# Optimization experiments

Measured on AMD Instinct MI355X. Metric: run time of the kernel, lower is better.

## Reference

```python
import jax, jax.numpy as jnp
import numpy as np

B, S, D, H = 2, 2048, 1024, 16
DK = D // H


def setup_inputs() -> dict:
    key = jax.random.key(0)
    ks = jax.random.split(key, 11)
    def lin(k):
        kw, kb = jax.random.split(k)
        bound = 1.0 / np.sqrt(D)
        w = jax.random.uniform(kw, (D, D), jnp.float32, -bound, bound)
        b = jax.random.uniform(kb, (D,), jnp.float32, -bound, bound)
        return w, b
    wq_w, wq_b = lin(ks[0])
    wk_w, wk_b = lin(ks[1])
    wv_w, wv_b = lin(ks[2])
    wo_w, wo_b = lin(ks[3])
    q = jax.random.normal(ks[4], (B, S, D), jnp.float32)
    k = jax.random.normal(ks[5], (B, S, D), jnp.float32)
    v = jax.random.normal(ks[6], (B, S, D), jnp.float32)
    # causal mask, broadcastable to (B, H, S, S); 0 -> masked
    mask = jnp.tril(jnp.ones((S, S), jnp.int32))[None, None, :, :]
    return {"q": q, "k": k, "v": v, "mask": mask,
            "wq_w": wq_w, "wq_b": wq_b, "wk_w": wk_w, "wk_b": wk_b,
            "wv_w": wv_w, "wv_b": wv_b, "wo_w": wo_w, "wo_b": wo_b}


def reference(q, k, v, mask, wq_w, wq_b, wk_w, wk_b, wv_w, wv_b, wo_w, wo_b):
    # projections (torch Linear: x @ W^T + b)
    def split_heads(x):  # (B,S,D) -> (B,H,S,DK)
        return x.reshape(B, S, H, DK).transpose(0, 2, 1, 3)
    Q = split_heads(q @ wq_w.T + wq_b)
    K = split_heads(k @ wk_w.T + wk_b)
    V = split_heads(v @ wv_w.T + wv_b)
    scores = jnp.einsum('bhqd,bhkd->bhqk', Q, K) / np.sqrt(DK).astype(np.float32)
    scores = jnp.where(mask == 0, jnp.float32(-1e9), scores)
    attn = jax.nn.softmax(scores, axis=-1)
    out = jnp.einsum('bhqk,bhkd->bhqd', attn, V)  # (B,H,S,DK)
    out = out.transpose(0, 2, 1, 3).reshape(B, S, D)
    return out @ wo_w.T + wo_b
```

## Files before the change

kernel.cpp:

```cpp
#include <hip/hip_runtime.h>

#define DEV __device__ __forceinline__

typedef __attribute__((ext_vector_type(8))) short short8;
typedef __attribute__((ext_vector_type(4))) float f32x4;
typedef __bf16 bf16x8 __attribute__((ext_vector_type(8)));
typedef unsigned int u32;
typedef unsigned short u16;

constexpr int Bb = 2, Ss = 2048, Dd = 1024, Hh = 16, DKc = 64;
constexpr int Kk = 1024;

#define QSCALE 0.1803368801111204f

DEV u16 f2bf(float f) {
  u32 u = __builtin_bit_cast(u32, f);
  u32 r = (u + 0x7fffu + ((u >> 16) & 1u)) >> 16;
  return (u16)r;
}

DEV u32 pk_bf16(float lo, float hi) {
  u32 w;
  asm("v_cvt_pk_bf16_f32 %0, %1, %2" : "=v"(w) : "v"(lo), "v"(hi));
  return w;
}

DEV f32x4 mfma16(short8 a, short8 b, f32x4 c) {
  return __builtin_amdgcn_mfma_f32_16x16x32_bf16(
      __builtin_bit_cast(bf16x8, a), __builtin_bit_cast(bf16x8, b), c, 0, 0, 0);
}

DEV void gload_lds16(const u16* g, u16* lds) {
  __builtin_amdgcn_global_load_lds(
      (const __attribute__((address_space(1))) u32*)g,
      (__attribute__((address_space(3))) u32*)lds, 16, 0, 0);
}

struct CvtArgs {
  const float* in[7];
  u16* out[7];
  int n[7];
};

__global__ __launch_bounds__(256) void cvt_all(CvtArgs a) {
  int z = blockIdx.z;
  int i = (blockIdx.x * 256 + threadIdx.x) * 4;
  if (i >= a.n[z]) return;
  float4 v = *reinterpret_cast<const float4*>(a.in[z] + i);
  ushort4 o;
  o.x = f2bf(v.x); o.y = f2bf(v.y); o.z = f2bf(v.z); o.w = f2bf(v.w);
  *reinterpret_cast<ushort4*>(a.out[z] + i) = o;
}

template<int MT, int NT>
DEV void gemm_core(const u16* __restrict__ A, const u16* __restrict__ Bt,
                   u16* smA, u16* smB, f32x4 (&acc)[MT][NT], int gm0, int gn0) {
  constexpr int NSTEP = Kk / 32;
  constexpr int SA = MT * 1024;
  constexpr int SB = NT * 1024;
  constexpr int S = MT / 2 + NT / 2;
  const int tid = threadIdx.x;
  const int w = tid >> 6, l = tid & 63;
  const int g = (l >> 4) & 3, r = l & 15;
  const int wm = w >> 1, wn = w & 1;
  const int srow = l >> 2, scol = (l & 3) * 8;

  auto stage = [&](int buf, int kt) {
    int kb = kt * 32;
#pragma unroll
    for (int cc = 0; cc < MT / 2; ++cc) {
      int c = w + cc * 4;
      gload_lds16(A + (size_t)(gm0 + c * 16 + srow) * Kk + kb + scol,
                  smA + buf * SA + c * 512);
    }
#pragma unroll
    for (int cc = 0; cc < NT / 2; ++cc) {
      int c = w + cc * 4;
      gload_lds16(Bt + (size_t)(gn0 + c * 16 + srow) * Kk + kb + scol,
                  smB + buf * SB + c * 512);
    }
  };

  stage(0, 0);
  stage(1, 1);
  for (int kt = 0; kt < NSTEP; ++kt) {
    const int buf = kt % 3;
    if (kt + 1 < NSTEP) {
      if constexpr (S == 4) asm volatile("s_waitcnt vmcnt(4)" ::: "memory");
      else                  asm volatile("s_waitcnt vmcnt(3)" ::: "memory");
    } else {
      asm volatile("s_waitcnt vmcnt(0)" ::: "memory");
    }
    __builtin_amdgcn_s_barrier();
    __builtin_amdgcn_sched_barrier(0);
    if (kt + 2 < NSTEP) stage((kt + 2) % 3, kt + 2);

    short8 af[MT], bf_[NT];
#pragma unroll
    for (int t = 0; t < MT; ++t)
      af[t] = *reinterpret_cast<const short8*>(
          smA + buf * SA + (wm * (MT * 16) + t * 16 + r) * 32 + g * 8);
#pragma unroll
    for (int t = 0; t < NT; ++t)
      bf_[t] = *reinterpret_cast<const short8*>(
          smB + buf * SB + (wn * (NT * 16) + t * 16 + r) * 32 + g * 8);
    __builtin_amdgcn_s_setprio(1);
#pragma unroll
    for (int mt = 0; mt < MT; ++mt)
#pragma unroll
      for (int nt = 0; nt < NT; ++nt)
        acc[mt][nt] = mfma16(af[mt], bf_[nt], acc[mt][nt]);
    __builtin_amdgcn_s_setprio(0);
  }
}

__global__ __launch_bounds__(256, 3) void proj_qkv(
    const u16* __restrict__ xq, const u16* __restrict__ xk, const u16* __restrict__ xv,
    const u16* __restrict__ Wq, const u16* __restrict__ Wk, const u16* __restrict__ Wv,
    const float* __restrict__ bq, const float* __restrict__ bk, const float* __restrict__ bv,
    u16* __restrict__ Qh, u16* __restrict__ Kh, u16* __restrict__ Vt) {
  __shared__ u16 smA[3 * 128 * 32], smB[3 * 128 * 32];
  const int flat = (blockIdx.z * 32 + blockIdx.y) * 8 + blockIdx.x;
  const int nid = (flat & 7) * 96 + (flat >> 3);
  const int bx = nid & 7, by = (nid >> 3) & 31, z = nid >> 8;
  const u16* A = z == 0 ? xq : (z == 1 ? xk : xv);
  const u16* W = z == 0 ? Wq : (z == 1 ? Wk : Wv);
  const float* bias = z == 0 ? bq : (z == 1 ? bk : bv);
  u16* out = z == 0 ? Qh : (z == 1 ? Kh : Vt);
  const float sc = z == 0 ? QSCALE : 1.0f;
  const int gm0 = by * 128, gn0 = bx * 128;
  f32x4 acc[4][4] = {};
  gemm_core<4, 4>(A, W, smA, smB, acc, gm0, gn0);

  const int tid = threadIdx.x;
  const int w = tid >> 6, l = tid & 63, g = (l >> 4) & 3, r = l & 15;
  const int wm = w >> 1, wn = w & 1;
#pragma unroll
  for (int mt = 0; mt < 4; ++mt) {
#pragma unroll
    for (int nt = 0; nt < 4; ++nt) {
      int ncol = gn0 + wn * 64 + nt * 16 + r;
      int h = ncol >> 6, dk = ncol & 63;
      float bb = bias[ncol];
      int mrow0 = gm0 + wm * 64 + mt * 16 + g * 4;
      int b = mrow0 >> 11, s0 = mrow0 & 2047;
      if (z < 2) {
#pragma unroll
        for (int i = 0; i < 4; ++i)
          out[(((size_t)b * Hh + h) * Ss + s0 + i) * DKc + dk] =
              f2bf((acc[mt][nt][i] + bb) * sc);
      } else {
        ushort4 ov;
        ov.x = f2bf(acc[mt][nt][0] + bb);
        ov.y = f2bf(acc[mt][nt][1] + bb);
        ov.z = f2bf(acc[mt][nt][2] + bb);
        ov.w = f2bf(acc[mt][nt][3] + bb);
        *reinterpret_cast<ushort4*>(
            &out[(((size_t)b * Hh + h) * DKc + dk) * Ss + s0]) = ov;
      }
    }
  }
}

__global__ __launch_bounds__(256, 2) void attn(
    const u16* __restrict__ Qh, const u16* __restrict__ Kh,
    const u16* __restrict__ Vt, u16* __restrict__ Ob) {
  __shared__ u16 smK[4][64 * 64];
  __shared__ u16 smV[4][64 * 64];
  __shared__ u16 smP[4][16 * 72];

  const int fid = blockIdx.y * 16 + blockIdx.x;
  const int xcd = fid & 7, slot = fid >> 3;
  const int bh = xcd * 4 + (slot >> 4);
  const int pair = slot & 15;
  const int bidx = bh >> 4, h = bh & 15;

  const int tid = threadIdx.x, w = tid >> 6, l = tid & 63;
  const int g = (l >> 4) & 3, r = l & 15;

  const u16* Qb = Qh + (size_t)bh * Ss * DKc;
  const u16* Kb = Kh + (size_t)bh * Ss * DKc;
  const u16* Vb = Vt + (size_t)bh * DKc * Ss;
  u16* Pw = smP[w];

  const int srow0 = tid >> 3, schunk = tid & 7;

  auto stage = [&](int sl, int kb) {
#pragma unroll
    for (int j = 0; j < 2; ++j) {
      int row = j * 32 + srow0;
      int c = schunk ^ (row & 7);
      u16* dK = smK[sl] + (j * 256 + w * 64) * 8;
      u16* dV = smV[sl] + (j * 256 + w * 64) * 8;
      gload_lds16(Kb + (size_t)(kb + row) * DKc + c * 8, dK);
      gload_lds16(Vb + (size_t)row * Ss + kb + c * 8, dV);
    }
  };

  for (int t2 = 0; t2 < 2; ++t2) {
    const int qt = (t2 == 0) ? (31 - pair) : pair;
    const int ntile = qt + 1;
    const int npair = (ntile + 1) >> 1;
    const int qw = qt * 64 + w * 16;
    const int q = qw + r;

    if (t2) __builtin_amdgcn_s_barrier();

    short8 qf[2];
    qf[0] = *reinterpret_cast<const short8*>(Qb + (size_t)q * DKc + g * 8);
    qf[1] = *reinterpret_cast<const short8*>(Qb + (size_t)q * DKc + 32 + g * 8);

    stage(0, 0);
    if (ntile > 1) stage(1, 64);

    f32x4 o[4] = {};
    float m_s = -3e38f, l_s = 0.f;

    for (int pp = 0; pp < npair; ++pp) {
      const int slotA = (pp & 1) * 2;
      const int kbA = pp * 128;
      const bool hasB = (2 * pp + 1 < ntile);
      const bool diagA = (2 * pp == qt);
      const bool diagB = hasB && (2 * pp + 1 == qt);

      asm volatile("s_waitcnt vmcnt(0)" ::: "memory");
      __builtin_amdgcn_s_barrier();
      __builtin_amdgcn_sched_barrier(0);
      if (pp + 1 < npair) {
        int nb = ((pp + 1) & 1) * 2;
        stage(nb, kbA + 128);
        if (2 * pp + 3 < ntile) stage(nb + 1, kbA + 192);
      }

      f32x4 sA[4] = {}, sB[4] = {};
      __builtin_amdgcn_s_setprio(1);
#pragma unroll
      for (int ks = 0; ks < 2; ++ks)
#pragma unroll
        for (int nt = 0; nt < 4; ++nt) {
          int row = nt * 16 + r;
          int ch = (ks * 4 + g) ^ (row & 7);
          short8 kf = *reinterpret_cast<const short8*>(&smK[slotA][row * 64 + ch * 8]);
          sA[nt] = mfma16(kf, qf[ks], sA[nt]);
        }
      if (hasB) {
#pragma unroll
        for (int ks = 0; ks < 2; ++ks)
#pragma unroll
          for (int nt = 0; nt < 4; ++nt) {
            int row = nt * 16 + r;
            int ch = (ks * 4 + g) ^ (row & 7);
            short8 kf = *reinterpret_cast<const short8*>(&smK[slotA + 1][row * 64 + ch * 8]);
            sB[nt] = mfma16(kf, qf[ks], sB[nt]);
          }
      }
      __builtin_amdgcn_s_setprio(0);

      const int qloc = w * 16 + r;
      if (diagA) {
#pragma unroll
        for (int nt = 0; nt < 4; ++nt)
#pragma unroll
          for (int i = 0; i < 4; ++i)
            if (nt * 16 + g * 4 + i > qloc) sA[nt][i] = -1e30f;
      }
      if (diagB) {
#pragma unroll
        for (int nt = 0; nt < 4; ++nt)
#pragma unroll
          for (int i = 0; i < 4; ++i)
            if (nt * 16 + g * 4 + i > qloc) sB[nt][i] = -1e30f;
      }

      float mx0 = fmaxf(fmaxf(sA[0][0], sA[0][1]), fmaxf(sA[0][2], sA[0][3]));
      float mx1 = fmaxf(fmaxf(sA[1][0], sA[1][1]), fmaxf(sA[1][2], sA[1][3]));
      float mx2 = fmaxf(fmaxf(sA[2][0], sA[2][1]), fmaxf(sA[2][2], sA[2][3]));
      float mx3 = fmaxf(fmaxf(sA[3][0], sA[3][1]), fmaxf(sA[3][2], sA[3][3]));
      float mx = fmaxf(fmaxf(mx0, mx1), fmaxf(mx2, mx3));
      if (hasB) {
        float nx0 = fmaxf(fmaxf(sB[0][0], sB[0][1]), fmaxf(sB[0][2], sB[0][3]));
        float nx1 = fmaxf(fmaxf(sB[1][0], sB[1][1]), fmaxf(sB[1][2], sB[1][3]));
        float nx2 = fmaxf(fmaxf(sB[2][0], sB[2][1]), fmaxf(sB[2][2], sB[2][3]));
        float nx3 = fmaxf(fmaxf(sB[3][0], sB[3][1]), fmaxf(sB[3][2], sB[3][3]));
        mx = fmaxf(mx, fmaxf(fmaxf(nx0, nx1), fmaxf(nx2, nx3)));
      }

      if (__any(mx > m_s + 8.f)) {
        float mr = fmaxf(mx, __shfl_xor(mx, 16));
        mr = fmaxf(mr, __shfl_xor(mr, 32));
        float mn = fmaxf(m_s, mr);
        float f = __builtin_amdgcn_exp2f(m_s - mn);
        m_s = mn;
        l_s *= f;
#pragma unroll
        for (int dt = 0; dt < 4; ++dt) {
          o[dt][0] *= f; o[dt][1] *= f; o[dt][2] *= f; o[dt][3] *= f;
        }
      }

#pragma unroll
      for (int nt = 0; nt < 4; ++nt) {
        float p0 = __builtin_amdgcn_exp2f(sA[nt][0] - m_s);
        float p1 = __builtin_amdgcn_exp2f(sA[nt][1] - m_s);
        float p2 = __builtin_amdgcn_exp2f(sA[nt][2] - m_s);
        float p3 = __builtin_amdgcn_exp2f(sA[nt][3] - m_s);
        l_s += (p0 + p1) + (p2 + p3);
        *reinterpret_cast<u32*>(&Pw[r * 72 + nt * 16 + g * 4])     = pk_bf16(p0, p1);
        *reinterpret_cast<u32*>(&Pw[r * 72 + nt * 16 + g * 4 + 2]) = pk_bf16(p2, p3);
      }
      __builtin_amdgcn_s_setprio(1);
#pragma unroll
      for (int ks = 0; ks < 2; ++ks) {
        short8 pf = *reinterpret_cast<const short8*>(&Pw[r * 72 + ks * 32 + g * 8]);
#pragma unroll
        for (int dt = 0; dt < 4; ++dt) {
          int row = dt * 16 + r;
          int ch = (ks * 4 + g) ^ (row & 7);
          short8 vf = *reinterpret_cast<const short8*>(&smV[slotA][row * 64 + ch * 8]);
          o[dt] = mfma16(vf, pf, o[dt]);
        }
      }
      __builtin_amdgcn_s_setprio(0);

      if (hasB) {
#pragma unroll
        for (int nt = 0; nt < 4; ++nt) {
          float p0 = __builtin_amdgcn_exp2f(sB[nt][0] - m_s);
          float p1 = __builtin_amdgcn_exp2f(sB[nt][1] - m_s);
          float p2 = __builtin_amdgcn_exp2f(sB[nt][2] - m_s);
          float p3 = __builtin_amdgcn_exp2f(sB[nt][3] - m_s);
          l_s += (p0 + p1) + (p2 + p3);
          *reinterpret_cast<u32*>(&Pw[r * 72 + nt * 16 + g * 4])     = pk_bf16(p0, p1);
          *reinterpret_cast<u32*>(&Pw[r * 72 + nt * 16 + g * 4 + 2]) = pk_bf16(p2, p3);
        }
        __builtin_amdgcn_s_setprio(1);
#pragma unroll
        for (int ks = 0; ks < 2; ++ks) {
          short8 pf = *reinterpret_cast<const short8*>(&Pw[r * 72 + ks * 32 + g * 8]);
#pragma unroll
          for (int dt = 0; dt < 4; ++dt) {
            int row = dt * 16 + r;
            int ch = (ks * 4 + g) ^ (row & 7);
            short8 vf = *reinterpret_cast<const short8*>(&smV[slotA + 1][row * 64 + ch * 8]);
            o[dt] = mfma16(vf, pf, o[dt]);
          }
        }
        __builtin_amdgcn_s_setprio(0);
      }
    }

    float lt = l_s;
    lt += __shfl_xor(lt, 16);
    lt += __shfl_xor(lt, 32);
    float inv = 1.f / lt;
    size_t ro = ((size_t)bidx * Ss + q) * Dd + h * DKc;
#pragma unroll
    for (int dt = 0; dt < 4; ++dt) {
      ushort4 ov;
      ov.x = f2bf(o[dt][0] * inv);
      ov.y = f2bf(o[dt][1] * inv);
      ov.z = f2bf(o[dt][2] * inv);
      ov.w = f2bf(o[dt][3] * inv);
      *reinterpret_cast<ushort4*>(&Ob[ro + dt * 16 + g * 4]) = ov;
    }
  }
}

__global__ __launch_bounds__(256, 2) void gemm_out(
    const u16* __restrict__ Ob, const u16* __restrict__ Wo,
    const float* __restrict__ bo, float* __restrict__ out) {
  __shared__ u16 smA[3 * 64 * 32], smB[3 * 128 * 32];
  const int flat = blockIdx.y * 8 + blockIdx.x;
  const int nid = (flat & 7) * 64 + (flat >> 3);
  const int bx = nid & 7, by = nid >> 3;
  const int gm0 = by * 64, gn0 = bx * 128;
  f32x4 acc[2][4] = {};
  gemm_core<2, 4>(Ob, Wo, smA, smB, acc, gm0, gn0);

  const int tid = threadIdx.x;
  const int w = tid >> 6, l = tid & 63, g = (l >> 4) & 3, r = l & 15;
  const int wm = w >> 1, wn = w & 1;
#pragma unroll
  for (int mt = 0; mt < 2; ++mt) {
#pragma unroll
    for (int nt = 0; nt < 4; ++nt) {
      int ncol = gn0 + wn * 64 + nt * 16 + r;
      float bb = bo[ncol];
#pragma unroll
      for (int i = 0; i < 4; ++i) {
        int mrow = gm0 + wm * 32 + mt * 16 + g * 4 + i;
        out[(size_t)mrow * Dd + ncol] = acc[mt][nt][i] + bb;
      }
    }
  }
}

extern "C" void kernel_launch(void* const* d_in, const int* in_sizes, int n_in,
                              void* d_out, int out_size, void* d_ws, size_t ws_size,
                              hipStream_t stream) {
  const float* q    = (const float*)d_in[0];
  const float* k    = (const float*)d_in[1];
  const float* v    = (const float*)d_in[2];
  const float* wq_w = (const float*)d_in[4];
  const float* wq_b = (const float*)d_in[5];
  const float* wk_w = (const float*)d_in[6];
  const float* wk_b = (const float*)d_in[7];
  const float* wv_w = (const float*)d_in[8];
  const float* wv_b = (const float*)d_in[9];
  const float* wo_w = (const float*)d_in[10];
  const float* wo_b = (const float*)d_in[11];

  char* ws = (char*)d_ws;
  u16* xq  = (u16*)(ws + 0);
  u16* xk  = (u16*)(ws + 8388608);
  u16* xv  = (u16*)(ws + 16777216);
  u16* Wqb = (u16*)(ws + 25165824);
  u16* Wkb = (u16*)(ws + 27262976);
  u16* Wvb = (u16*)(ws + 29360128);
  u16* Wob = (u16*)(ws + 31457280);
  u16* Qh  = (u16*)(ws + 33554432);
  u16* Kh  = (u16*)(ws + 41943040);
  u16* Vt  = (u16*)(ws + 50331648);
  u16* Ob  = (u16*)(ws + 0);

  CvtArgs ca;
  ca.in[0] = q;    ca.out[0] = xq;  ca.n[0] = 4194304;
  ca.in[1] = k;    ca.out[1] = xk;  ca.n[1] = 4194304;
  ca.in[2] = v;    ca.out[2] = xv;  ca.n[2] = 4194304;
  ca.in[3] = wq_w; ca.out[3] = Wqb; ca.n[3] = 1048576;
  ca.in[4] = wk_w; ca.out[4] = Wkb; ca.n[4] = 1048576;
  ca.in[5] = wv_w; ca.out[5] = Wvb; ca.n[5] = 1048576;
  ca.in[6] = wo_w; ca.out[6] = Wob; ca.n[6] = 1048576;

  cvt_all<<<dim3(4096, 1, 7), 256, 0, stream>>>(ca);
  proj_qkv<<<dim3(8, 32, 3), 256, 0, stream>>>(xq, xk, xv, Wqb, Wkb, Wvb,
                                               wq_b, wk_b, wv_b, Qh, Kh, Vt);
  attn<<<dim3(16, 32), 256, 0, stream>>>(Qh, Kh, Vt, Ob);
  gemm_out<<<dim3(8, 64), 256, 0, stream>>>(Ob, Wob, wo_b, (float*)d_out);
}
```

Baseline: 112.7 us.

## Process 128 query rows per attention block sharing K/V tiles, split K/V staging

```diff
diff --git a/kernel.cpp b/kernel.cpp
--- a/kernel.cpp
+++ b/kernel.cpp
@@ -4,6 +4,7 @@
 
 typedef __attribute__((ext_vector_type(8))) short short8;
 typedef __attribute__((ext_vector_type(4))) float f32x4;
+typedef __attribute__((ext_vector_type(4))) unsigned int u32x4;
 typedef __bf16 bf16x8 __attribute__((ext_vector_type(8)));
 typedef unsigned int u32;
 typedef unsigned short u16;
@@ -34,6 +35,14 @@
   __builtin_amdgcn_global_load_lds(
       (const __attribute__((address_space(1))) u32*)g,
       (__attribute__((address_space(3))) u32*)lds, 16, 0, 0);
+}
+
+DEV float tree16(const f32x4 (&s)[4]) {
+  float a = fmaxf(fmaxf(s[0][0], s[0][1]), fmaxf(s[0][2], s[0][3]));
+  float b = fmaxf(fmaxf(s[1][0], s[1][1]), fmaxf(s[1][2], s[1][3]));
+  float c = fmaxf(fmaxf(s[2][0], s[2][1]), fmaxf(s[2][2], s[2][3]));
+  float d = fmaxf(fmaxf(s[3][0], s[3][1]), fmaxf(s[3][2], s[3][3]));
+  return fmaxf(fmaxf(a, b), fmaxf(c, d));
 }
 
 struct CvtArgs {
@@ -165,14 +174,12 @@
 __global__ __launch_bounds__(256, 2) void attn(
     const u16* __restrict__ Qh, const u16* __restrict__ Kh,
     const u16* __restrict__ Vt, u16* __restrict__ Ob) {
-  __shared__ u16 smK[4][64 * 64];
-  __shared__ u16 smV[4][64 * 64];
-  __shared__ u16 smP[4][16 * 72];
-
-  const int fid = blockIdx.y * 16 + blockIdx.x;
-  const int xcd = fid & 7, slot = fid >> 3;
-  const int bh = xcd * 4 + (slot >> 4);
-  const int pair = slot & 15;
+  __shared__ u16 smK[2][64 * 64];
+  __shared__ u16 smV[2][64 * 64];
+  __shared__ u16 smP[4][32 * 76];
+
+  const int bh = blockIdx.x;
+  const int j = 15 - blockIdx.y;
   const int bidx = bh >> 4, h = bh & 15;
 
   const int tid = threadIdx.x, w = tid >> 6, l = tid & 63;
@@ -185,184 +192,180 @@
 
   const int srow0 = tid >> 3, schunk = tid & 7;
 
-  auto stage = [&](int sl, int kb) {
-#pragma unroll
-    for (int j = 0; j < 2; ++j) {
-      int row = j * 32 + srow0;
+  auto stageK = [&](int sl, int kb) {
+#pragma unroll
+    for (int jj = 0; jj < 2; ++jj) {
+      int row = jj * 32 + srow0;
       int c = schunk ^ (row & 7);
-      u16* dK = smK[sl] + (j * 256 + w * 64) * 8;
-      u16* dV = smV[sl] + (j * 256 + w * 64) * 8;
-      gload_lds16(Kb + (size_t)(kb + row) * DKc + c * 8, dK);
-      gload_lds16(Vb + (size_t)row * Ss + kb + c * 8, dV);
+      gload_lds16(Kb + (size_t)(kb + row) * DKc + c * 8,
+                  smK[sl] + (jj * 256 + w * 64) * 8);
     }
   };
-
-  for (int t2 = 0; t2 < 2; ++t2) {
-    const int qt = (t2 == 0) ? (31 - pair) : pair;
-    const int ntile = qt + 1;
-    const int npair = (ntile + 1) >> 1;
-    const int qw = qt * 64 + w * 16;
-    const int q = qw + r;
-
-    if (t2) __builtin_amdgcn_s_barrier();
-
-    short8 qf[2];
-    qf[0] = *reinterpret_cast<const short8*>(Qb + (size_t)q * DKc + g * 8);
-    qf[1] = *reinterpret_cast<const short8*>(Qb + (size_t)q * DKc + 32 + g * 8);
-
-    stage(0, 0);
-    if (ntile > 1) stage(1, 64);
-
-    f32x4 o[4] = {};
-    float m_s = -3e38f, l_s = 0.f;
-
-    for (int pp = 0; pp < npair; ++pp) {
-      const int slotA = (pp & 1) * 2;
-      const int kbA = pp * 128;
-      const bool hasB = (2 * pp + 1 < ntile);
-      const bool diagA = (2 * pp == qt);
-      const bool diagB = hasB && (2 * pp + 1 == qt);
-
-      asm volatile("s_waitcnt vmcnt(0)" ::: "memory");
-      __builtin_amdgcn_s_barrier();
-      __builtin_amdgcn_sched_barrier(0);
-      if (pp + 1 < npair) {
-        int nb = ((pp + 1) & 1) * 2;
-        stage(nb, kbA + 128);
-        if (2 * pp + 3 < ntile) stage(nb + 1, kbA + 192);
+  auto stageV = [&](int sl, int kb) {
+#pragma unroll
+    for (int jj = 0; jj < 2; ++jj) {
+      int row = jj * 32 + srow0;
+      int c = schunk ^ (row & 7);
+      gload_lds16(Vb + (size_t)row * Ss + kb + c * 8,
+                  smV[sl] + (jj * 256 + w * 64) * 8);
+    }
+  };
+
+  const int q0 = j * 128;
+  const int npair = j + 1;
+  const int qX = q0 + w * 16 + r;
+  const int qY = qX + 64;
+
+  short8 qfX[2], qfY[2];
+  qfX[0] = *reinterpret_cast<const short8*>(Qb + (size_t)qX * DKc + g * 8);
+  qfX[1] = *reinterpret_cast<const short8*>(Qb + (size_t)qX * DKc + 32 + g * 8);
+  qfY[0] = *reinterpret_cast<const short8*>(Qb + (size_t)qY * DKc + g * 8);
+  qfY[1] = *reinterpret_cast<const short8*>(Qb + (size_t)qY * DKc + 32 + g * 8);
+
+  stageK(0, 0); stageK(1, 64);
+  stageV(0, 0); stageV(1, 64);
+
+  f32x4 oX[4] = {}, oY[4] = {};
+  float mX = -3e38f, lX = 0.f, mY = -3e38f, lY = 0.f;
+
+  auto emitP = [&](f32x4 (&s)[4], float m, float& lacc, int pr) {
+#pragma unroll
+    for (int nt = 0; nt < 4; ++nt) {
+      float p0 = __builtin_amdgcn_exp2f(s[nt][0] - m);
+      float p1 = __builtin_amdgcn_exp2f(s[nt][1] - m);
+      float p2 = __builtin_amdgcn_exp2f(s[nt][2] - m);
+      float p3 = __builtin_amdgcn_exp2f(s[nt][3] - m);
+      lacc += (p0 + p1) + (p2 + p3);
+      *reinterpret_cast<u32*>(&Pw[pr * 76 + nt * 16 + g * 4])     = pk_bf16(p0, p1);
+      *reinterpret_cast<u32*>(&Pw[pr * 76 + nt * 16 + g * 4 + 2]) = pk_bf16(p2, p3);
+    }
+  };
+  auto pv = [&](const u16* smv, int pr, f32x4 (&o)[4]) {
+#pragma unroll
+    for (int ks = 0; ks < 2; ++ks) {
+      short8 pf = *reinterpret_cast<const short8*>(&Pw[pr * 76 + ks * 32 + g * 8]);
+#pragma unroll
+      for (int dt = 0; dt < 4; ++dt) {
+        int row = dt * 16 + r;
+        int ch = (ks * 4 + g) ^ (row & 7);
+        short8 vf = *reinterpret_cast<const short8*>(&smv[row * 64 + ch * 8]);
+        o[dt] = mfma16(vf, pf, o[dt]);
       }
-
-      f32x4 sA[4] = {}, sB[4] = {};
-      __builtin_amdgcn_s_setprio(1);
+    }
+  };
+
+  for (int pp = 0; pp < npair; ++pp) {
+    const int kbA = pp * 128;
+    const bool last = (pp + 1 == npair);
+
+    asm volatile("s_waitcnt vmcnt(4)" ::: "memory");
+    __builtin_amdgcn_s_barrier();
+    __builtin_amdgcn_sched_barrier(0);
+
+    f32x4 sXA[4] = {}, sXB[4] = {}, sYA[4] = {}, sYB[4] = {};
+    __builtin_amdgcn_s_setprio(1);
+#pragma unroll
+    for (int ks = 0; ks < 2; ++ks)
+#pragma unroll
+      for (int nt = 0; nt < 4; ++nt) {
+        int row = nt * 16 + r;
+        int ch = (ks * 4 + g) ^ (row & 7);
+        short8 kf = *reinterpret_cast<const short8*>(&smK[0][row * 64 + ch * 8]);
+        sXA[nt] = mfma16(kf, qfX[ks], sXA[nt]);
+        sYA[nt] = mfma16(kf, qfY[ks], sYA[nt]);
+      }
+    if (!last) {
 #pragma unroll
       for (int ks = 0; ks < 2; ++ks)
 #pragma unroll
         for (int nt = 0; nt < 4; ++nt) {
           int row = nt * 16 + r;
           int ch = (ks * 4 + g) ^ (row & 7);
-          short8 kf = *reinterpret_cast<const short8*>(&smK[slotA][row * 64 + ch * 8]);
-          sA[nt] = mfma16(kf, qf[ks], sA[nt]);
+          short8 kf = *reinterpret_cast<const short8*>(&smK[1][row * 64 + ch * 8]);
+          sXB[nt] = mfma16(kf, qfX[ks], sXB[nt]);
+          sYB[nt] = mfma16(kf, qfY[ks], sYB[nt]);
         }
-      if (hasB) {
-#pragma unroll
-        for (int ks = 0; ks < 2; ++ks)
-#pragma unroll
-          for (int nt = 0; nt < 4; ++nt) {
-            int row = nt * 16 + r;
-            int ch = (ks * 4 + g) ^ (row & 7);
-            short8 kf = *reinterpret_cast<const short8*>(&smK[slotA + 1][row * 64 + ch * 8]);
-            sB[nt] = mfma16(kf, qf[ks], sB[nt]);
-          }
+    } else {
+#pragma unroll
+      for (int ks = 0; ks < 2; ++ks)
+#pragma unroll
+        for (int nt = 0; nt < 4; ++nt) {
+          int row = nt * 16 + r;
+          int ch = (ks * 4 + g) ^ (row & 7);
+          short8 kf = *reinterpret_cast<const short8*>(&smK[1][row * 64 + ch * 8]);
+          sYB[nt] = mfma16(kf, qfY[ks], sYB[nt]);
+        }
+    }
+    __builtin_amdgcn_s_setprio(0);
+
+    asm volatile("s_waitcnt vmcnt(0)" ::: "memory");
+    __builtin_amdgcn_s_barrier();
+    __builtin_amdgcn_sched_barrier(0);
+    if (pp + 1 < npair) { stageK(0, kbA + 128); stageK(1, kbA + 192); }
+
+    if (last) {
+      const int qloc = w * 16 + r;
+#pragma unroll
+      for (int nt = 0; nt < 4; ++nt)
+#pragma unroll
+        for (int i = 0; i < 4; ++i)
+          if (nt * 16 + g * 4 + i > qloc) { sXA[nt][i] = -1e30f; sYB[nt][i] = -1e30f; }
+    }
+
+    float mxX = tree16(sXA);
+    if (!last) mxX = fmaxf(mxX, tree16(sXB));
+    float mxY = fmaxf(tree16(sYA), tree16(sYB));
+
+    if (__any(fmaxf(mxX - mX, mxY - mY) > 8.f)) {
+      float mrX = fmaxf(mxX, __shfl_xor(mxX, 16));
+      mrX = fmaxf(mrX, __shfl_xor(mrX, 32));
+      float mrY = fmaxf(mxY, __shfl_xor(mxY, 16));
+      mrY = fmaxf(mrY, __shfl_xor(mrY, 32));
+      float mnX = fmaxf(mX, mrX), mnY = fmaxf(mY, mrY);
+      float fX = __builtin_amdgcn_exp2f(mX - mnX);
+      float fY = __builtin_amdgcn_exp2f(mY - mnY);
+      mX = mnX; mY = mnY; lX *= fX; lY *= fY;
+#pragma unroll
+      for (int dt = 0; dt < 4; ++dt) {
+        oX[dt][0] *= fX; oX[dt][1] *= fX; oX[dt][2] *= fX; oX[dt][3] *= fX;
+        oY[dt][0] *= fY; oY[dt][1] *= fY; oY[dt][2] *= fY; oY[dt][3] *= fY;
       }
-      __builtin_amdgcn_s_setprio(0);
-
-      const int qloc = w * 16 + r;
-      if (diagA) {
-#pragma unroll
-        for (int nt = 0; nt < 4; ++nt)
-#pragma unroll
-          for (int i = 0; i < 4; ++i)
-            if (nt * 16 + g * 4 + i > qloc) sA[nt][i] = -1e30f;
-      }
-      if (diagB) {
-#pragma unroll
-        for (int nt = 0; nt < 4; ++nt)
-#pragma unroll
-          for (int i = 0; i < 4; ++i)
-            if (nt * 16 + g * 4 + i > qloc) sB[nt][i] = -1e30f;
-      }
-
-      float mx0 = fmaxf(fmaxf(sA[0][0], sA[0][1]), fmaxf(sA[0][2], sA[0][3]));
-      float mx1 = fmaxf(fmaxf(sA[1][0], sA[1][1]), fmaxf(sA[1][2], sA[1][3]));
-      float mx2 = fmaxf(fmaxf(sA[2][0], sA[2][1]), fmaxf(sA[2][2], sA[2][3]));
-      float mx3 = fmaxf(fmaxf(sA[3][0], sA[3][1]), fmaxf(sA[3][2], sA[3][3]));
-      float mx = fmaxf(fmaxf(mx0, mx1), fmaxf(mx2, mx3));
-      if (hasB) {
-        float nx0 = fmaxf(fmaxf(sB[0][0], sB[0][1]), fmaxf(sB[0][2], sB[0][3]));
-        float nx1 = fmaxf(fmaxf(sB[1][0], sB[1][1]), fmaxf(sB[1][2], sB[1][3]));
-        float nx2 = fmaxf(fmaxf(sB[2][0], sB[2][1]), fmaxf(sB[2][2], sB[2][3]));
-        float nx3 = fmaxf(fmaxf(sB[3][0], sB[3][1]), fmaxf(sB[3][2], sB[3][3]));
-        mx = fmaxf(mx, fmaxf(fmaxf(nx0, nx1), fmaxf(nx2, nx3)));
-      }
-
-      if (__any(mx > m_s + 8.f)) {
-        float mr = fmaxf(mx, __shfl_xor(mx, 16));
-        mr = fmaxf(mr, __shfl_xor(mr, 32));
-        float mn = fmaxf(m_s, mr);
-        float f = __builtin_amdgcn_exp2f(m_s - mn);
-        m_s = mn;
-        l_s *= f;
-#pragma unroll
-        for (int dt = 0; dt < 4; ++dt) {
-          o[dt][0] *= f; o[dt][1] *= f; o[dt][2] *= f; o[dt][3] *= f;
-        }
-      }
-
-#pragma unroll
-      for (int nt = 0; nt < 4; ++nt) {
-        float p0 = __builtin_amdgcn_exp2f(sA[nt][0] - m_s);
-        float p1 = __builtin_amdgcn_exp2f(sA[nt][1] - m_s);
-        float p2 = __builtin_amdgcn_exp2f(sA[nt][2] - m_s);
-        float p3 = __builtin_amdgcn_exp2f(sA[nt][3] - m_s);
-        l_s += (p0 + p1) + (p2 + p3);
-        *reinterpret_cast<u32*>(&Pw[r * 72 + nt * 16 + g * 4])     = pk_bf16(p0, p1);
-        *reinterpret_cast<u32*>(&Pw[r * 72 + nt * 16 + g * 4 + 2]) = pk_bf16(p2, p3);
-      }
-      __builtin_amdgcn_s_setprio(1);
-#pragma unroll
-      for (int ks = 0; ks < 2; ++ks) {
-        short8 pf = *reinterpret_cast<const short8*>(&Pw[r * 72 + ks * 32 + g * 8]);
-#pragma unroll
-        for (int dt = 0; dt < 4; ++dt) {
-          int row = dt * 16 + r;
-          int ch = (ks * 4 + g) ^ (row & 7);
-          short8 vf = *reinterpret_cast<const short8*>(&smV[slotA][row * 64 + ch * 8]);
-          o[dt] = mfma16(vf, pf, o[dt]);
-        }
-      }
-      __builtin_amdgcn_s_setprio(0);
-
-      if (hasB) {
-#pragma unroll
-        for (int nt = 0; nt < 4; ++nt) {
-          float p0 = __builtin_amdgcn_exp2f(sB[nt][0] - m_s);
-          float p1 = __builtin_amdgcn_exp2f(sB[nt][1] - m_s);
-          float p2 = __builtin_amdgcn_exp2f(sB[nt][2] - m_s);
-          float p3 = __builtin_amdgcn_exp2f(sB[nt][3] - m_s);
-          l_s += (p0 + p1) + (p2 + p3);
-          *reinterpret_cast<u32*>(&Pw[r * 72 + nt * 16 + g * 4])     = pk_bf16(p0, p1);
-          *reinterpret_cast<u32*>(&Pw[r * 72 + nt * 16 + g * 4 + 2]) = pk_bf16(p2, p3);
-        }
-        __builtin_amdgcn_s_setprio(1);
-#pragma unroll
-        for (int ks = 0; ks < 2; ++ks) {
-          short8 pf = *reinterpret_cast<const short8*>(&Pw[r * 72 + ks * 32 + g * 8]);
-#pragma unroll
-          for (int dt = 0; dt < 4; ++dt) {
-            int row = dt * 16 + r;
-            int ch = (ks * 4 + g) ^ (row & 7);
-            short8 vf = *reinterpret_cast<const short8*>(&smV[slotA + 1][row * 64 + ch * 8]);
-            o[dt] = mfma16(vf, pf, o[dt]);
-          }
-        }
-        __builtin_amdgcn_s_setprio(0);
-      }
-    }
-
-    float lt = l_s;
-    lt += __shfl_xor(lt, 16);
-    lt += __shfl_xor(lt, 32);
-    float inv = 1.f / lt;
-    size_t ro = ((size_t)bidx * Ss + q) * Dd + h * DKc;
-#pragma unroll
-    for (int dt = 0; dt < 4; ++dt) {
-      ushort4 ov;
-      ov.x = f2bf(o[dt][0] * inv);
-      ov.y = f2bf(o[dt][1] * inv);
-      ov.z = f2bf(o[dt][2] * inv);
-      ov.w = f2bf(o[dt][3] * inv);
-      *reinterpret_cast<ushort4*>(&Ob[ro + dt * 16 + g * 4]) = ov;
-    }
+    }
+
+    emitP(sXA, mX, lX, r);
+    emitP(sYA, mY, lY, 16 + r);
+    __builtin_amdgcn_s_setprio(1);
+    pv(smV[0], r, oX);
+    pv(smV[0], 16 + r, oY);
+    __builtin_amdgcn_s_setprio(0);
+
+    if (!last) emitP(sXB, mX, lX, r);
+    emitP(sYB, mY, lY, 16 + r);
+    __builtin_amdgcn_s_setprio(1);
+    if (!last) pv(smV[1], r, oX);
+    pv(smV[1], 16 + r, oY);
+    __builtin_amdgcn_s_setprio(0);
+
+    __builtin_amdgcn_s_barrier();
+    if (pp + 1 < npair) { stageV(0, kbA + 128); stageV(1, kbA + 192); }
+  }
+
+  float tX = lX;
+  tX += __shfl_xor(tX, 16); tX += __shfl_xor(tX, 32);
+  float tY = lY;
+  tY += __shfl_xor(tY, 16); tY += __shfl_xor(tY, 32);
+  float invX = 1.f / tX, invY = 1.f / tY;
+  size_t roX = ((size_t)bidx * Ss + qX) * Dd + h * DKc;
+  size_t roY = ((size_t)bidx * Ss + qY) * Dd + h * DKc;
+#pragma unroll
+  for (int dt = 0; dt < 4; ++dt) {
+    ushort4 ovX, ovY;
+    ovX.x = f2bf(oX[dt][0] * invX); ovX.y = f2bf(oX[dt][1] * invX);
+    ovX.z = f2bf(oX[dt][2] * invX); ovX.w = f2bf(oX[dt][3] * invX);
+    ovY.x = f2bf(oY[dt][0] * invY); ovY.y = f2bf(oY[dt][1] * invY);
+    ovY.z = f2bf(oY[dt][2] * invY); ovY.w = f2bf(oY[dt][3] * invY);
+    *reinterpret_cast<ushort4*>(&Ob[roX + dt * 16 + g * 4]) = ovX;
+    *reinterpret_cast<ushort4*>(&Ob[roY + dt * 16 + g * 4]) = ovY;
   }
 }
 
@@ -371,8 +374,8 @@
     const float* __restrict__ bo, float* __restrict__ out) {
   __shared__ u16 smA[3 * 64 * 32], smB[3 * 128 * 32];
   const int flat = blockIdx.y * 8 + blockIdx.x;
-  const int nid = (flat & 7) * 64 + (flat >> 3);
-  const int bx = nid & 7, by = nid >> 3;
+  const int by = (flat & 7) * 8 + ((flat >> 3) & 7);
+  const int bx = flat >> 6;
   const int gm0 = by * 64, gn0 = bx * 128;
   f32x4 acc[2][4] = {};
   gemm_core<2, 4>(Ob, Wo, smA, smB, acc, gm0, gn0);
@@ -435,6 +438,6 @@
   cvt_all<<<dim3(4096, 1, 7), 256, 0, stream>>>(ca);
   proj_qkv<<<dim3(8, 32, 3), 256, 0, stream>>>(xq, xk, xv, Wqb, Wkb, Wvb,
                                                wq_b, wk_b, wv_b, Qh, Kh, Vt);
-  attn<<<dim3(16, 32), 256, 0, stream>>>(Qh, Kh, Vt, Ob);
+  attn<<<dim3(32, 16), 256, 0, stream>>>(Qh, Kh, Vt, Ob);
   gemm_out<<<dim3(8, 64), 256, 0, stream>>>(Ob, Wob, wo_b, (float*)d_out);
 }
```

Result: slower. 129.2 us (+14.7%).

## Restructure attention to one query tile per block with split K/V staging

Applied to the files above, without the earlier changes.

```diff
diff --git a/kernel.cpp b/kernel.cpp
--- a/kernel.cpp
+++ b/kernel.cpp
@@ -4,6 +4,7 @@
 
 typedef __attribute__((ext_vector_type(8))) short short8;
 typedef __attribute__((ext_vector_type(4))) float f32x4;
+typedef __attribute__((ext_vector_type(4))) unsigned int u32x4;
 typedef __bf16 bf16x8 __attribute__((ext_vector_type(8)));
 typedef unsigned int u32;
 typedef unsigned short u16;
@@ -162,17 +163,15 @@
   }
 }
 
-__global__ __launch_bounds__(256, 2) void attn(
+__global__ __launch_bounds__(256, 3) void attn(
     const u16* __restrict__ Qh, const u16* __restrict__ Kh,
     const u16* __restrict__ Vt, u16* __restrict__ Ob) {
-  __shared__ u16 smK[4][64 * 64];
-  __shared__ u16 smV[4][64 * 64];
-  __shared__ u16 smP[4][16 * 72];
-
-  const int fid = blockIdx.y * 16 + blockIdx.x;
-  const int xcd = fid & 7, slot = fid >> 3;
-  const int bh = xcd * 4 + (slot >> 4);
-  const int pair = slot & 15;
+  __shared__ u16 smK[2][64 * 64];
+  __shared__ u16 smV[2][64 * 64];
+  __shared__ u16 smP[4][16 * 76];
+
+  const int bh = blockIdx.x;
+  const int qt = 31 - blockIdx.y;
   const int bidx = bh >> 4, h = bh & 15;
 
   const int tid = threadIdx.x, w = tid >> 6, l = tid & 63;
@@ -185,184 +184,199 @@
 
   const int srow0 = tid >> 3, schunk = tid & 7;
 
-  auto stage = [&](int sl, int kb) {
+  auto stageK = [&](int sl, int kb) {
 #pragma unroll
     for (int j = 0; j < 2; ++j) {
       int row = j * 32 + srow0;
       int c = schunk ^ (row & 7);
-      u16* dK = smK[sl] + (j * 256 + w * 64) * 8;
-      u16* dV = smV[sl] + (j * 256 + w * 64) * 8;
-      gload_lds16(Kb + (size_t)(kb + row) * DKc + c * 8, dK);
-      gload_lds16(Vb + (size_t)row * Ss + kb + c * 8, dV);
+      gload_lds16(Kb + (size_t)(kb + row) * DKc + c * 8,
+                  smK[sl] + (j * 256 + w * 64) * 8);
     }
   };
-
-  for (int t2 = 0; t2 < 2; ++t2) {
-    const int qt = (t2 == 0) ? (31 - pair) : pair;
-    const int ntile = qt + 1;
-    const int npair = (ntile + 1) >> 1;
-    const int qw = qt * 64 + w * 16;
-    const int q = qw + r;
-
-    if (t2) __builtin_amdgcn_s_barrier();
-
-    short8 qf[2];
-    qf[0] = *reinterpret_cast<const short8*>(Qb + (size_t)q * DKc + g * 8);
-    qf[1] = *reinterpret_cast<const short8*>(Qb + (size_t)q * DKc + 32 + g * 8);
-
-    stage(0, 0);
-    if (ntile > 1) stage(1, 64);
-
-    f32x4 o[4] = {};
-    float m_s = -3e38f, l_s = 0.f;
-
-    for (int pp = 0; pp < npair; ++pp) {
-      const int slotA = (pp & 1) * 2;
-      const int kbA = pp * 128;
-      const bool hasB = (2 * pp + 1 < ntile);
-      const bool diagA = (2 * pp == qt);
-      const bool diagB = hasB && (2 * pp + 1 == qt);
-
-      asm volatile("s_waitcnt vmcnt(0)" ::: "memory");
-      __builtin_amdgcn_s_barrier();
-      __builtin_amdgcn_sched_barrier(0);
-      if (pp + 1 < npair) {
-        int nb = ((pp + 1) & 1) * 2;
-        stage(nb, kbA + 128);
-        if (2 * pp + 3 < ntile) stage(nb + 1, kbA + 192);
-      }
-
-      f32x4 sA[4] = {}, sB[4] = {};
-      __builtin_amdgcn_s_setprio(1);
+  auto stageV = [&](int sl, int kb) {
+#pragma unroll
+    for (int j = 0; j < 2; ++j) {
+      int row = j * 32 + srow0;
+      int c = schunk ^ (row & 7);
+      gload_lds16(Vb + (size_t)row * Ss + kb + c * 8,
+                  smV[sl] + (j * 256 + w * 64) * 8);
+    }
+  };
+
+  const int ntile = qt + 1;
+  const int npair = (ntile + 1) >> 1;
+  const int qw = qt * 64 + w * 16;
+  const int q = qw + r;
+
+  short8 qf[2];
+  qf[0] = *reinterpret_cast<const short8*>(Qb + (size_t)q * DKc + g * 8);
+  qf[1] = *reinterpret_cast<const short8*>(Qb + (size_t)q * DKc + 32 + g * 8);
+
+  {
+    int kb1 = (ntile > 1) ? 64 : 0;
+    stageK(0, 0); stageK(1, kb1);
+    stageV(0, 0); stageV(1, kb1);
+  }
+
+  f32x4 o[4] = {};
+  float m_s = -3e38f, l_s = 0.f;
+
+  for (int pp = 0; pp < npair; ++pp) {
+    const int kbA = pp * 128;
+    const bool hasB = (2 * pp + 1 < ntile);
+    const bool diagA = (2 * pp == qt);
+    const bool diagB = hasB && (2 * pp + 1 == qt);
+
+    asm volatile("s_waitcnt vmcnt(4)" ::: "memory");
+    __builtin_amdgcn_s_barrier();
+    __builtin_amdgcn_sched_barrier(0);
+
+    f32x4 sA[4] = {}, sB[4] = {};
+    __builtin_amdgcn_s_setprio(1);
+#pragma unroll
+    for (int ks = 0; ks < 2; ++ks)
+#pragma unroll
+      for (int nt = 0; nt < 4; ++nt) {
+        int row = nt * 16 + r;
+        int ch = (ks * 4 + g) ^ (row & 7);
+        short8 kf = *reinterpret_cast<const short8*>(&smK[0][row * 64 + ch * 8]);
+        sA[nt] = mfma16(kf, qf[ks], sA[nt]);
+      }
+    if (hasB) {
 #pragma unroll
       for (int ks = 0; ks < 2; ++ks)
 #pragma unroll
         for (int nt = 0; nt < 4; ++nt) {
           int row = nt * 16 + r;
           int ch = (ks * 4 + g) ^ (row & 7);
-          short8 kf = *reinterpret_cast<const short8*>(&smK[slotA][row * 64 + ch * 8]);
-          sA[nt] = mfma16(kf, qf[ks], sA[nt]);
+          short8 kf = *reinterpret_cast<const short8*>(&smK[1][row * 64 + ch * 8]);
+          sB[nt] = mfma16(kf, qf[ks], sB[nt]);
         }
-      if (hasB) {
-#pragma unroll
-        for (int ks = 0; ks < 2; ++ks)
-#pragma unroll
-          for (int nt = 0; nt < 4; ++nt) {
-            int row = nt * 16 + r;
-            int ch = (ks * 4 + g) ^ (row & 7);
-            short8 kf = *reinterpret_cast<const short8*>(&smK[slotA + 1][row * 64 + ch * 8]);
-            sB[nt] = mfma16(kf, qf[ks], sB[nt]);
-          }
-      }
-      __builtin_amdgcn_s_setprio(0);
-
-      const int qloc = w * 16 + r;
-      if (diagA) {
-#pragma unroll
-        for (int nt = 0; nt < 4; ++nt)
-#pragma unroll
-          for (int i = 0; i < 4; ++i)
-            if (nt * 16 + g * 4 + i > qloc) sA[nt][i] = -1e30f;
-      }
-      if (diagB) {
-#pragma unroll
-        for (int nt = 0; nt < 4; ++nt)
-#pragma unroll
-          for (int i = 0; i < 4; ++i)
-            if (nt * 16 + g * 4 + i > qloc) sB[nt][i] = -1e30f;
-      }
-
-      float mx0 = fmaxf(fmaxf(sA[0][0], sA[0][1]), fmaxf(sA[0][2], sA[0][3]));
-      float mx1 = fmaxf(fmaxf(sA[1][0], sA[1][1]), fmaxf(sA[1][2], sA[1][3]));
-      float mx2 = fmaxf(fmaxf(sA[2][0], sA[2][1]), fmaxf(sA[2][2], sA[2][3]));
-      float mx3 = fmaxf(fmaxf(sA[3][0], sA[3][1]), fmaxf(sA[3][2], sA[3][3]));
-      float mx = fmaxf(fmaxf(mx0, mx1), fmaxf(mx2, mx3));
-      if (hasB) {
-        float nx0 = fmaxf(fmaxf(sB[0][0], sB[0][1]), fmaxf(sB[0][2], sB[0][3]));
-        float nx1 = fmaxf(fmaxf(sB[1][0], sB[1][1]), fmaxf(sB[1][2], sB[1][3]));
-        float nx2 = fmaxf(fmaxf(sB[2][0], sB[2][1]), fmaxf(sB[2][2], sB[2][3]));
-        float nx3 = fmaxf(fmaxf(sB[3][0], sB[3][1]), fmaxf(sB[3][2], sB[3][3]));
-        mx = fmaxf(mx, fmaxf(fmaxf(nx0, nx1), fmaxf(nx2, nx3)));
-      }
-
-      if (__any(mx > m_s + 8.f)) {
-        float mr = fmaxf(mx, __shfl_xor(mx, 16));
-        mr = fmaxf(mr, __shfl_xor(mr, 32));
-        float mn = fmaxf(m_s, mr);
-        float f = __builtin_amdgcn_exp2f(m_s - mn);
-        m_s = mn;
-        l_s *= f;
-#pragma unroll
-        for (int dt = 0; dt < 4; ++dt) {
-          o[dt][0] *= f; o[dt][1] *= f; o[dt][2] *= f; o[dt][3] *= f;
-        }
-      }
-
+    }
+    __builtin_amdgcn_s_setprio(0);
+
+    asm volatile("s_waitcnt vmcnt(0)" ::: "memory");
+    __builtin_amdgcn_s_barrier();
+    __builtin_amdgcn_sched_barrier(0);
+    if (pp + 1 < npair) {
+      int nkb = kbA + 128;
+      int nkb1 = (2 * pp + 3 < ntile) ? nkb + 64 : nkb;
+      stageK(0, nkb); stageK(1, nkb1);
+    }
+
+    const int qloc = w * 16 + r;
+    if (diagA) {
+#pragma unroll
+      for (int nt = 0; nt < 4; ++nt)
+#pragma unroll
+        for (int i = 0; i < 4; ++i)
+          if (nt * 16 + g * 4 + i > qloc) sA[nt][i] = -1e30f;
+    }
+    if (diagB) {
+#pragma unroll
+      for (int nt = 0; nt < 4; ++nt)
+#pragma unroll
+        for (int i = 0; i < 4; ++i)
+          if (nt * 16 + g * 4 + i > qloc) sB[nt][i] = -1e30f;
+    }
+
+    float mx0 = fmaxf(fmaxf(sA[0][0], sA[0][1]), fmaxf(sA[0][2], sA[0][3]));
+    float mx1 = fmaxf(fmaxf(sA[1][0], sA[1][1]), fmaxf(sA[1][2], sA[1][3]));
+    float mx2 = fmaxf(fmaxf(sA[2][0], sA[2][1]), fmaxf(sA[2][2], sA[2][3]));
+    float mx3 = fmaxf(fmaxf(sA[3][0], sA[3][1]), fmaxf(sA[3][2], sA[3][3]));
+    float mx = fmaxf(fmaxf(mx0, mx1), fmaxf(mx2, mx3));
+    if (hasB) {
+      float nx0 = fmaxf(fmaxf(sB[0][0], sB[0][1]), fmaxf(sB[0][2], sB[0][3]));
+      float nx1 = fmaxf(fmaxf(sB[1][0], sB[1][1]), fmaxf(sB[1][2], sB[1][3]));
+      float nx2 = fmaxf(fmaxf(sB[2][0], sB[2][1]), fmaxf(sB[2][2], sB[2][3]));
+      float nx3 = fmaxf(fmaxf(sB[3][0], sB[3][1]), fmaxf(sB[3][2], sB[3][3]));
+      mx = fmaxf(mx, fmaxf(fmaxf(nx0, nx1), fmaxf(nx2, nx3)));
+    }
+
+    if (__any(mx > m_s + 8.f)) {
+      float mr = fmaxf(mx, __shfl_xor(mx, 16));
+      mr = fmaxf(mr, __shfl_xor(mr, 32));
+      float mn = fmaxf(m_s, mr);
+      float f = __builtin_amdgcn_exp2f(m_s - mn);
+      m_s = mn;
+      l_s *= f;
+#pragma unroll
+      for (int dt = 0; dt < 4; ++dt) {
+        o[dt][0] *= f; o[dt][1] *= f; o[dt][2] *= f; o[dt][3] *= f;
+      }
+    }
+
+#pragma unroll
+    for (int nt = 0; nt < 4; ++nt) {
+      float p0 = __builtin_amdgcn_exp2f(sA[nt][0] - m_s);
+      float p1 = __builtin_amdgcn_exp2f(sA[nt][1] - m_s);
+      float p2 = __builtin_amdgcn_exp2f(sA[nt][2] - m_s);
+      float p3 = __builtin_amdgcn_exp2f(sA[nt][3] - m_s);
+      l_s += (p0 + p1) + (p2 + p3);
+      *reinterpret_cast<u32*>(&Pw[r * 76 + nt * 16 + g * 4])     = pk_bf16(p0, p1);
+      *reinterpret_cast<u32*>(&Pw[r * 76 + nt * 16 + g * 4 + 2]) = pk_bf16(p2, p3);
+    }
+    __builtin_amdgcn_s_setprio(1);
+#pragma unroll
+    for (int ks = 0; ks < 2; ++ks) {
+      short8 pf = *reinterpret_cast<const short8*>(&Pw[r * 76 + ks * 32 + g * 8]);
+#pragma unroll
+      for (int dt = 0; dt < 4; ++dt) {
+        int row = dt * 16 + r;
+        int ch = (ks * 4 + g) ^ (row & 7);
+        short8 vf = *reinterpret_cast<const short8*>(&smV[0][row * 64 + ch * 8]);
+        o[dt] = mfma16(vf, pf, o[dt]);
+      }
+    }
+    __builtin_amdgcn_s_setprio(0);
+
+    if (hasB) {
 #pragma unroll
       for (int nt = 0; nt < 4; ++nt) {
-        float p0 = __builtin_amdgcn_exp2f(sA[nt][0] - m_s);
-        float p1 = __builtin_amdgcn_exp2f(sA[nt][1] - m_s);
-        float p2 = __builtin_amdgcn_exp2f(sA[nt][2] - m_s);
-        float p3 = __builtin_amdgcn_exp2f(sA[nt][3] - m_s);
+        float p0 = __builtin_amdgcn_exp2f(sB[nt][0] - m_s);
+        float p1 = __builtin_amdgcn_exp2f(sB[nt][1] - m_s);
+        float p2 = __builtin_amdgcn_exp2f(sB[nt][2] - m_s);
+        float p3 = __builtin_amdgcn_exp2f(sB[nt][3] - m_s);
         l_s += (p0 + p1) + (p2 + p3);
-        *reinterpret_cast<u32*>(&Pw[r * 72 + nt * 16 + g * 4])     = pk_bf16(p0, p1);
-        *reinterpret_cast<u32*>(&Pw[r * 72 + nt * 16 + g * 4 + 2]) = pk_bf16(p2, p3);
+        *reinterpret_cast<u32*>(&Pw[r * 76 + nt * 16 + g * 4])     = pk_bf16(p0, p1);
+        *reinterpret_cast<u32*>(&Pw[r * 76 + nt * 16 + g * 4 + 2]) = pk_bf16(p2, p3);
       }
       __builtin_amdgcn_s_setprio(1);
 #pragma unroll
       for (int ks = 0; ks < 2; ++ks) {
-        short8 pf = *reinterpret_cast<const short8*>(&Pw[r * 72 + ks * 32 + g * 8]);
+        short8 pf = *reinterpret_cast<const short8*>(&Pw[r * 76 + ks * 32 + g * 8]);
 #pragma unroll
         for (int dt = 0; dt < 4; ++dt) {
           int row = dt * 16 + r;
           int ch = (ks * 4 + g) ^ (row & 7);
-          short8 vf = *reinterpret_cast<const short8*>(&smV[slotA][row * 64 + ch * 8]);
+          short8 vf = *reinterpret_cast<const short8*>(&smV[1][row * 64 + ch * 8]);
           o[dt] = mfma16(vf, pf, o[dt]);
         }
       }
       __builtin_amdgcn_s_setprio(0);
-
-      if (hasB) {
-#pragma unroll
-        for (int nt = 0; nt < 4; ++nt) {
-          float p0 = __builtin_amdgcn_exp2f(sB[nt][0] - m_s);
-          float p1 = __builtin_amdgcn_exp2f(sB[nt][1] - m_s);
-          float p2 = __builtin_amdgcn_exp2f(sB[nt][2] - m_s);
-          float p3 = __builtin_amdgcn_exp2f(sB[nt][3] - m_s);
-          l_s += (p0 + p1) + (p2 + p3);
-          *reinterpret_cast<u32*>(&Pw[r * 72 + nt * 16 + g * 4])     = pk_bf16(p0, p1);
-          *reinterpret_cast<u32*>(&Pw[r * 72 + nt * 16 + g * 4 + 2]) = pk_bf16(p2, p3);
-        }
-        __builtin_amdgcn_s_setprio(1);
-#pragma unroll
-        for (int ks = 0; ks < 2; ++ks) {
-          short8 pf = *reinterpret_cast<const short8*>(&Pw[r * 72 + ks * 32 + g * 8]);
-#pragma unroll
-          for (int dt = 0; dt < 4; ++dt) {
-            int row = dt * 16 + r;
-            int ch = (ks * 4 + g) ^ (row & 7);
-            short8 vf = *reinterpret_cast<const short8*>(&smV[slotA + 1][row * 64 + ch * 8]);
-            o[dt] = mfma16(vf, pf, o[dt]);
-          }
-        }
-        __builtin_amdgcn_s_setprio(0);
-      }
-    }
-
-    float lt = l_s;
-    lt += __shfl_xor(lt, 16);
-    lt += __shfl_xor(lt, 32);
-    float inv = 1.f / lt;
-    size_t ro = ((size_t)bidx * Ss + q) * Dd + h * DKc;
-#pragma unroll
-    for (int dt = 0; dt < 4; ++dt) {
-      ushort4 ov;
-      ov.x = f2bf(o[dt][0] * inv);
-      ov.y = f2bf(o[dt][1] * inv);
-      ov.z = f2bf(o[dt][2] * inv);
-      ov.w = f2bf(o[dt][3] * inv);
-      *reinterpret_cast<ushort4*>(&Ob[ro + dt * 16 + g * 4]) = ov;
-    }
+    }
+
+    __builtin_amdgcn_s_barrier();
+    if (pp + 1 < npair) {
+      int nkb = kbA + 128;
+      int nkb1 = (2 * pp + 3 < ntile) ? nkb + 64 : nkb;
+      stageV(0, nkb); stageV(1, nkb1);
+    }
+  }
+
+  float lt = l_s;
+  lt += __shfl_xor(lt, 16);
+  lt += __shfl_xor(lt, 32);
+  float inv = 1.f / lt;
+  size_t ro = ((size_t)bidx * Ss + q) * Dd + h * DKc;
+#pragma unroll
+  for (int dt = 0; dt < 4; ++dt) {
+    ushort4 ov;
+    ov.x = f2bf(o[dt][0] * inv);
+    ov.y = f2bf(o[dt][1] * inv);
+    ov.z = f2bf(o[dt][2] * inv);
+    ov.w = f2bf(o[dt][3] * inv);
+    *reinterpret_cast<ushort4*>(&Ob[ro + dt * 16 + g * 4]) = ov;
   }
 }
 
@@ -371,8 +385,8 @@
     const float* __restrict__ bo, float* __restrict__ out) {
   __shared__ u16 smA[3 * 64 * 32], smB[3 * 128 * 32];
   const int flat = blockIdx.y * 8 + blockIdx.x;
-  const int nid = (flat & 7) * 64 + (flat >> 3);
-  const int bx = nid & 7, by = nid >> 3;
+  const int by = (flat & 7) * 8 + ((flat >> 3) & 7);
+  const int bx = flat >> 6;
   const int gm0 = by * 64, gn0 = bx * 128;
   f32x4 acc[2][4] = {};
   gemm_core<2, 4>(Ob, Wo, smA, smB, acc, gm0, gn0);
@@ -435,6 +449,6 @@
   cvt_all<<<dim3(4096, 1, 7), 256, 0, stream>>>(ca);
   proj_qkv<<<dim3(8, 32, 3), 256, 0, stream>>>(xq, xk, xv, Wqb, Wkb, Wvb,
                                                wq_b, wk_b, wv_b, Qh, Kh, Vt);
-  attn<<<dim3(16, 32), 256, 0, stream>>>(Qh, Kh, Vt, Ob);
+  attn<<<dim3(32, 32), 256, 0, stream>>>(Qh, Kh, Vt, Ob);
   gemm_out<<<dim3(8, 64), 256, 0, stream>>>(Ob, Wob, wo_b, (float*)d_out);
 }
```

New measurement: 120.5 us. 1.07x slower.

## Enlarge QKV projection tiles to 256x256 with 512-thread blocks and reorder out-GEMM blocks

Applied to the files above, without the earlier changes.

```diff
diff --git a/kernel.cpp b/kernel.cpp
--- a/kernel.cpp
+++ b/kernel.cpp
@@ -114,35 +114,85 @@
   }
 }
 
-__global__ __launch_bounds__(256, 3) void proj_qkv(
+__global__ __launch_bounds__(512, 1) void proj_qkv(
     const u16* __restrict__ xq, const u16* __restrict__ xk, const u16* __restrict__ xv,
     const u16* __restrict__ Wq, const u16* __restrict__ Wk, const u16* __restrict__ Wv,
     const float* __restrict__ bq, const float* __restrict__ bk, const float* __restrict__ bv,
     u16* __restrict__ Qh, u16* __restrict__ Kh, u16* __restrict__ Vt) {
-  __shared__ u16 smA[3 * 128 * 32], smB[3 * 128 * 32];
-  const int flat = (blockIdx.z * 32 + blockIdx.y) * 8 + blockIdx.x;
-  const int nid = (flat & 7) * 96 + (flat >> 3);
-  const int bx = nid & 7, by = (nid >> 3) & 31, z = nid >> 8;
+  __shared__ u16 smA[3 * 8192], smB[3 * 8192];
+  constexpr int NSTEP = Kk / 32;
+  const int flat = (blockIdx.z * 16 + blockIdx.y) * 4 + blockIdx.x;
+  const int nid = (flat & 7) * 24 + (flat >> 3);
+  const int bx = nid & 3, by = (nid >> 2) & 15, z = nid >> 6;
   const u16* A = z == 0 ? xq : (z == 1 ? xk : xv);
   const u16* W = z == 0 ? Wq : (z == 1 ? Wk : Wv);
   const float* bias = z == 0 ? bq : (z == 1 ? bk : bv);
   u16* out = z == 0 ? Qh : (z == 1 ? Kh : Vt);
   const float sc = z == 0 ? QSCALE : 1.0f;
-  const int gm0 = by * 128, gn0 = bx * 128;
-  f32x4 acc[4][4] = {};
-  gemm_core<4, 4>(A, W, smA, smB, acc, gm0, gn0);
+  const int gm0 = by * 256, gn0 = bx * 256;
 
   const int tid = threadIdx.x;
-  const int w = tid >> 6, l = tid & 63, g = (l >> 4) & 3, r = l & 15;
-  const int wm = w >> 1, wn = w & 1;
-#pragma unroll
-  for (int mt = 0; mt < 4; ++mt) {
+  const int w = tid >> 6, l = tid & 63;
+  const int g = (l >> 4) & 3, r = l & 15;
+  const int wm = w >> 2, wn = w & 3;
+
+  const int scs = tid & 3;
+
+  auto stage = [&](int buf, int kt) {
+    int kb = kt * 32;
+#pragma unroll
+    for (int j = 0; j < 2; ++j) {
+      int row = j * 128 + (tid >> 2);
+      int c = (scs ^ (row >> 1)) & 3;
+      gload_lds16(A + (size_t)(gm0 + row) * Kk + kb + c * 8,
+                  smA + buf * 8192 + (j * 512 + tid) * 8);
+      gload_lds16(W + (size_t)(gn0 + row) * Kk + kb + c * 8,
+                  smB + buf * 8192 + (j * 512 + tid) * 8);
+    }
+  };
+
+  f32x4 acc[8][4] = {};
+
+  stage(0, 0);
+  stage(1, 1);
+  for (int kt = 0; kt < NSTEP; ++kt) {
+    const int buf = kt % 3;
+    if (kt + 1 < NSTEP) asm volatile("s_waitcnt vmcnt(4)" ::: "memory");
+    else                asm volatile("s_waitcnt vmcnt(0)" ::: "memory");
+    __builtin_amdgcn_s_barrier();
+    __builtin_amdgcn_sched_barrier(0);
+    if (kt + 2 < NSTEP) stage((kt + 2) % 3, kt + 2);
+
+    short8 af[8], bf_[4];
+#pragma unroll
+    for (int t = 0; t < 8; ++t) {
+      int row = wm * 128 + t * 16 + r;
+      int ch = (g ^ (row >> 1)) & 3;
+      af[t] = *reinterpret_cast<const short8*>(smA + buf * 8192 + row * 32 + ch * 8);
+    }
+#pragma unroll
+    for (int t = 0; t < 4; ++t) {
+      int row = wn * 64 + t * 16 + r;
+      int ch = (g ^ (row >> 1)) & 3;
+      bf_[t] = *reinterpret_cast<const short8*>(smB + buf * 8192 + row * 32 + ch * 8);
+    }
+    __builtin_amdgcn_s_setprio(1);
+#pragma unroll
+    for (int mt = 0; mt < 8; ++mt)
+#pragma unroll
+      for (int nt = 0; nt < 4; ++nt)
+        acc[mt][nt] = mfma16(af[mt], bf_[nt], acc[mt][nt]);
+    __builtin_amdgcn_s_setprio(0);
+  }
+
+#pragma unroll
+  for (int mt = 0; mt < 8; ++mt) {
 #pragma unroll
     for (int nt = 0; nt < 4; ++nt) {
       int ncol = gn0 + wn * 64 + nt * 16 + r;
       int h = ncol >> 6, dk = ncol & 63;
       float bb = bias[ncol];
-      int mrow0 = gm0 + wm * 64 + mt * 16 + g * 4;
+      int mrow0 = gm0 + wm * 128 + mt * 16 + g * 4;
       int b = mrow0 >> 11, s0 = mrow0 & 2047;
       if (z < 2) {
 #pragma unroll
@@ -371,8 +421,8 @@
     const float* __restrict__ bo, float* __restrict__ out) {
   __shared__ u16 smA[3 * 64 * 32], smB[3 * 128 * 32];
   const int flat = blockIdx.y * 8 + blockIdx.x;
-  const int nid = (flat & 7) * 64 + (flat >> 3);
-  const int bx = nid & 7, by = nid >> 3;
+  const int by = (flat & 7) * 8 + ((flat >> 3) & 7);
+  const int bx = flat >> 6;
   const int gm0 = by * 64, gn0 = bx * 128;
   f32x4 acc[2][4] = {};
   gemm_core<2, 4>(Ob, Wo, smA, smB, acc, gm0, gn0);
@@ -433,7 +483,7 @@
   ca.in[6] = wo_w; ca.out[6] = Wob; ca.n[6] = 1048576;
 
   cvt_all<<<dim3(4096, 1, 7), 256, 0, stream>>>(ca);
-  proj_qkv<<<dim3(8, 32, 3), 256, 0, stream>>>(xq, xk, xv, Wqb, Wkb, Wvb,
+  proj_qkv<<<dim3(4, 16, 3), 512, 0, stream>>>(xq, xk, xv, Wqb, Wkb, Wvb,
                                                wq_b, wk_b, wv_b, Qh, Kh, Vt);
   attn<<<dim3(16, 32), 256, 0, stream>>>(Qh, Kh, Vt, Ob);
   gemm_out<<<dim3(8, 64), 256, 0, stream>>>(Ob, Wob, wo_b, (float*)d_out);
```

Measured after the change: 125.8 us. 11.6% more time.
